# Kernel optimization log

Measured on AMD Instinct MI355X. Metric: run time of the kernel, lower is better.

Reference implementation:

```python
import jax, jax.numpy as jnp
import numpy as np

N_NODES = 100000
N_EDGES = 300000
D = 256
N_LAYERS = 9
LN_EPS = 1e-5


def _mlp(h, w1, b1, w2, b2, ln_g, ln_b):
    # torch Linear: y = x @ W.T + b ; W is [out, in]
    h = jax.nn.relu(jnp.einsum('nd,hd->nh', h, w1) + b1)
    h = jnp.einsum('nh,oh->no', h, w2) + b2
    mu = jnp.mean(h, axis=-1, keepdims=True)
    var = jnp.mean(jnp.square(h - mu), axis=-1, keepdims=True)
    return (h - mu) * jax.lax.rsqrt(var + LN_EPS) * ln_g + ln_b


def setup_inputs() -> dict:
    key = jax.random.key(0)
    ks = jax.random.split(key, 16)
    s = 0.05  # small init scale for numerical sanity across 9 layers
    inp = {
        'x': jax.random.normal(ks[0], (N_NODES, D), dtype=jnp.float32),
        'edge_attr': jax.random.normal(ks[1], (N_EDGES, D), dtype=jnp.float32),
        'edge_fc1_w': jax.random.normal(ks[2], (N_LAYERS, D, D), dtype=jnp.float32) * s,
        'edge_fc1_b': jnp.zeros((N_LAYERS, D), dtype=jnp.float32),
        'edge_fc2_w': jax.random.normal(ks[3], (N_LAYERS, D, D), dtype=jnp.float32) * s,
        'edge_fc2_b': jnp.zeros((N_LAYERS, D), dtype=jnp.float32),
        'edge_ln_g': jnp.ones((N_LAYERS, D), dtype=jnp.float32),
        'edge_ln_b': jnp.zeros((N_LAYERS, D), dtype=jnp.float32),
        'node_fc1_w': jax.random.normal(ks[4], (N_LAYERS, D, D), dtype=jnp.float32) * s,
        'node_fc1_b': jnp.zeros((N_LAYERS, D), dtype=jnp.float32),
        'node_fc2_w': jax.random.normal(ks[5], (N_LAYERS, D, D), dtype=jnp.float32) * s,
        'node_fc2_b': jnp.zeros((N_LAYERS, D), dtype=jnp.float32),
        'node_ln_g': jnp.ones((N_LAYERS, D), dtype=jnp.float32),
        'node_ln_b': jnp.zeros((N_LAYERS, D), dtype=jnp.float32),
        'edge_index': jax.random.randint(ks[6], (2, N_EDGES), 0, N_NODES, dtype=jnp.int32),
    }
    return inp


def reference(x, edge_attr, edge_fc1_w, edge_fc1_b, edge_fc2_w, edge_fc2_b,
              edge_ln_g, edge_ln_b, node_fc1_w, node_fc1_b, node_fc2_w, node_fc2_b,
              node_ln_g, node_ln_b, edge_index):
    src = edge_index[0]  # x_j
    tgt = edge_index[1]  # aggregation target (aggr='add')
    for l in range(N_LAYERS):
        # edge MLP is applied to the ORIGINAL edge_attr in every layer
        e = _mlp(edge_attr, edge_fc1_w[l], edge_fc1_b[l], edge_fc2_w[l], edge_fc2_b[l],
                 edge_ln_g[l], edge_ln_b[l])
        msg = x[src] + e                               # [E, D] gather + add
        aggr = jax.ops.segment_sum(msg, tgt, num_segments=N_NODES)  # scatter-add
        upd = _mlp(aggr, node_fc1_w[l], node_fc1_b[l], node_fc2_w[l], node_fc2_b[l],
                   node_ln_g[l], node_ln_b[l])
        x = upd + x                                    # residual
    return x
```

## Files before the change

### kernel.cpp

```cpp
#include <hip/hip_runtime.h>
#include <stdint.h>

#define DD 256
#define NEDGE 300000
#define NNODE 100000
#define NLAY 9
#define LN_EPS 1e-5f

typedef __attribute__((ext_vector_type(8))) short bf16x8;
typedef __attribute__((ext_vector_type(4))) short s16x4;
typedef __attribute__((ext_vector_type(4))) float f32x4;
typedef __attribute__((ext_vector_type(4))) int i32x4;

static __device__ __forceinline__ short f2bf(float f) {
  union { float f; uint32_t u; } v; v.f = f;
  uint32_t r = (v.u + 0x7FFFu + ((v.u >> 16) & 1u)) >> 16;
  return (short)(uint16_t)r;
}
static __device__ __forceinline__ float bf2f(short s) {
  union { uint32_t u; float f; } v; v.u = ((uint32_t)(uint16_t)s) << 16;
  return v.f;
}
static __device__ __forceinline__ int addbf2(int a, int b) {
  const float a0 = bf2f((short)(a & 0xffff)), a1 = bf2f((short)(((uint32_t)a) >> 16));
  const float b0 = bf2f((short)(b & 0xffff)), b1 = bf2f((short)(((uint32_t)b) >> 16));
  const uint16_t r0 = (uint16_t)f2bf(a0 + b0), r1 = (uint16_t)f2bf(a1 + b1);
  return (int)(((uint32_t)r1 << 16) | r0);
}

static __device__ __forceinline__ void gld16(const void* g, void* l) {
  __builtin_amdgcn_global_load_lds((const __attribute__((address_space(1))) void*)g,
                                   (__attribute__((address_space(3))) void*)l, 16, 0, 0);
}

__global__ void cvtw_kernel(const float* __restrict__ src, short* __restrict__ dst, int nmat) {
  const int total = nmat * 8192;
  for (int j = blockIdx.x * blockDim.x + threadIdx.x; j < total; j += gridDim.x * blockDim.x) {
    const int m = j >> 13;
    const int jj = j & 8191;
    const int col = jj & 255;
    const int kq = jj >> 8;
    const float* s = src + (size_t)m * 65536 + col * 256 + kq * 8;
    const f32x4 u0 = *(const f32x4*)(s);
    const f32x4 u1 = *(const f32x4*)(s + 4);
    bf16x8 o;
#pragma unroll
    for (int q = 0; q < 4; ++q) { o[q] = f2bf(u0[q]); o[q + 4] = f2bf(u1[q]); }
    *(bf16x8*)(dst + (size_t)j * 8) = o;
  }
}

template<bool A_BF16, bool NODE>
__global__ __launch_bounds__(512, 4) void mlp_kernel(
    const void* __restrict__ Ain, const int* __restrict__ rowmap,
    const short* __restrict__ W1t, const short* __restrict__ W2t,
    const float* __restrict__ B1, const float* __restrict__ B2,
    const float* __restrict__ LG, const float* __restrict__ LB,
    short* __restrict__ OutB, float* __restrict__ OutF,
    short* __restrict__ XbOut, int M) {
  extern __shared__ char smem[];
  char* Abuf = smem + 32768;
  float* redbuf = (float*)(smem + 65536);
  const int tid = threadIdx.x;
  const int lane = tid & 63;
  const int wv = tid >> 6;
  const int wm = wv >> 2, wn = wv & 3;
  const int l15 = lane & 15, lq = lane >> 4;
  const int cbase = wn * 64;
  const int r0 = blockIdx.x * 64;

  auto stageW = [&](const short* Wt, int s, int slot) {
#pragma unroll
    for (int j = 0; j < 2; ++j) {
      const int c = tid + 512 * j;
      gld16(Wt + ((size_t)s * 1024 + c) * 8, smem + slot * 16384 + c * 16);
    }
  };

  if (A_BF16) {
    const short* A = (const short*)Ain;
#pragma unroll
    for (int j = 0; j < 4; ++j) {
      const int c = tid + 512 * j;
      const int row = c & 63, kq = c >> 6;
      const int gr = min(r0 + row, M - 1);
      gld16(A + (size_t)gr * DD + kq * 8, Abuf + c * 16);
    }
  } else {
    const float* A = (const float*)Ain;
#pragma unroll
    for (int j = 0; j < 4; ++j) {
      const int c = tid + 512 * j;
      const int row = c & 63, kq = c >> 6;
      const int gr0 = min(r0 + row, M - 1);
      const int gr = rowmap ? rowmap[gr0] : gr0;
      const f32x4 u0 = *(const f32x4*)(A + (size_t)gr * DD + kq * 8);
      const f32x4 u1 = *(const f32x4*)(A + (size_t)gr * DD + kq * 8 + 4);
      bf16x8 o;
#pragma unroll
      for (int q = 0; q < 4; ++q) { o[q] = f2bf(u0[q]); o[q + 4] = f2bf(u1[q]); }
      *(bf16x8*)(Abuf + c * 16) = o;
    }
  }
  stageW(W1t, 0, 0);
  __syncthreads();

  f32x4 acc[2][4];
#pragma unroll
  for (int mi = 0; mi < 2; ++mi)
#pragma unroll
    for (int ni = 0; ni < 4; ++ni) acc[mi][ni] = (f32x4){0.f, 0.f, 0.f, 0.f};

#pragma unroll
  for (int s = 0; s < 8; ++s) {
    if (s < 7) stageW(W1t, s + 1, (s + 1) & 1);
    else       stageW(W2t, 0, 0);
    const char* wb = smem + (s & 1) * 16384;
    bf16x8 a[2], b[4];
#pragma unroll
    for (int mi = 0; mi < 2; ++mi)
      a[mi] = *(const bf16x8*)(Abuf + (((s * 4 + lq) * 64) + wm * 32 + mi * 16 + l15) * 16);
#pragma unroll
    for (int ni = 0; ni < 4; ++ni)
      b[ni] = *(const bf16x8*)(wb + lq * 4096 + (cbase + ni * 16 + l15) * 16);
#pragma unroll
    for (int ni = 0; ni < 4; ++ni)
#pragma unroll
      for (int mi = 0; mi < 2; ++mi)
        acc[mi][ni] = __builtin_amdgcn_mfma_f32_16x16x32_bf16(b[ni], a[mi], acc[mi][ni], 0, 0, 0);
    __syncthreads();
  }

  short* hid = (short*)Abuf;
  {
    f32x4 b1q[4];
#pragma unroll
    for (int ni = 0; ni < 4; ++ni)
      b1q[ni] = *(const f32x4*)(B1 + cbase + ni * 16 + lq * 4);
#pragma unroll
    for (int mi = 0; mi < 2; ++mi) {
      const int r = wm * 32 + mi * 16 + l15;
#pragma unroll
      for (int ni = 0; ni < 4; ++ni) {
        const int c4 = cbase + ni * 16 + lq * 4;
        s16x4 o;
#pragma unroll
        for (int i = 0; i < 4; ++i) {
          o[i] = f2bf(fmaxf(acc[mi][ni][i] + b1q[ni][i], 0.f));
          acc[mi][ni][i] = 0.f;
        }
        *(s16x4*)((char*)hid + r * 512 + (((c4 >> 3) ^ (r & 7)) << 4) + (c4 & 7) * 2) = o;
      }
    }
  }
  __syncthreads();

#pragma unroll
  for (int s = 0; s < 8; ++s) {
    if (s < 7) stageW(W2t, s + 1, (s + 1) & 1);
    const char* wb = smem + (s & 1) * 16384;
    bf16x8 a[2], b[4];
#pragma unroll
    for (int mi = 0; mi < 2; ++mi) {
      const int r = wm * 32 + mi * 16 + l15;
      a[mi] = *(const bf16x8*)((const char*)hid + r * 512 + ((((s * 4 + lq)) ^ (r & 7)) << 4));
    }
#pragma unroll
    for (int ni = 0; ni < 4; ++ni)
      b[ni] = *(const bf16x8*)(wb + lq * 4096 + (cbase + ni * 16 + l15) * 16);
#pragma unroll
    for (int ni = 0; ni < 4; ++ni)
#pragma unroll
      for (int mi = 0; mi < 2; ++mi)
        acc[mi][ni] = __builtin_amdgcn_mfma_f32_16x16x32_bf16(b[ni], a[mi], acc[mi][ni], 0, 0, 0);
    __syncthreads();
  }

  f32x4 b2q[4];
#pragma unroll
  for (int ni = 0; ni < 4; ++ni)
    b2q[ni] = *(const f32x4*)(B2 + cbase + ni * 16 + lq * 4);
  float mean_[2], inv_[2];
#pragma unroll
  for (int mi = 0; mi < 2; ++mi) {
    float s1 = 0.f, s2 = 0.f;
#pragma unroll
    for (int ni = 0; ni < 4; ++ni)
#pragma unroll
      for (int i = 0; i < 4; ++i) {
        const float v = acc[mi][ni][i] + b2q[ni][i];
        s1 += v; s2 += v * v;
      }
    s1 += __shfl_xor(s1, 16); s2 += __shfl_xor(s2, 16);
    s1 += __shfl_xor(s1, 32); s2 += __shfl_xor(s2, 32);
    mean_[mi] = s1; inv_[mi] = s2;
  }
  if (lq == 0) {
#pragma unroll
    for (int mi = 0; mi < 2; ++mi) {
      const int r = wm * 32 + mi * 16 + l15;
      redbuf[(r * 4 + wn) * 2 + 0] = mean_[mi];
      redbuf[(r * 4 + wn) * 2 + 1] = inv_[mi];
    }
  }
  __syncthreads();
#pragma unroll
  for (int mi = 0; mi < 2; ++mi) {
    const int r = wm * 32 + mi * 16 + l15;
    float t1 = 0.f, t2 = 0.f;
#pragma unroll
    for (int w = 0; w < 4; ++w) {
      t1 += redbuf[(r * 4 + w) * 2 + 0];
      t2 += redbuf[(r * 4 + w) * 2 + 1];
    }
    const float mean = t1 * (1.f / 256.f);
    const float var = t2 * (1.f / 256.f) - mean * mean;
    mean_[mi] = mean;
    inv_[mi] = rsqrtf(var + LN_EPS);
  }

  f32x4 gq[4], bq[4];
#pragma unroll
  for (int ni = 0; ni < 4; ++ni) {
    gq[ni] = *(const f32x4*)(LG + cbase + ni * 16 + lq * 4);
    bq[ni] = *(const f32x4*)(LB + cbase + ni * 16 + lq * 4);
  }

  if (NODE) {
    const bool wantF = (OutF != nullptr);
    if (!wantF) {
      short* ob = (short*)Abuf;
#pragma unroll
      for (int mi = 0; mi < 2; ++mi) {
        const int r = wm * 32 + mi * 16 + l15;
#pragma unroll
        for (int ni = 0; ni < 4; ++ni) {
          const int c4 = cbase + ni * 16 + lq * 4;
          s16x4 o;
#pragma unroll
          for (int i = 0; i < 4; ++i)
            o[i] = f2bf((acc[mi][ni][i] + b2q[ni][i] - mean_[mi]) * inv_[mi] * gq[ni][i] + bq[ni][i]);
          *(s16x4*)((char*)ob + r * 512 + (((c4 >> 3) ^ (r & 7)) << 4) + (c4 & 7) * 2) = o;
        }
      }
      __syncthreads();
#pragma unroll
      for (int j = 0; j < 4; ++j) {
        const int gg = tid + 512 * j;
        const int row = gg >> 5, Lg = gg & 31;
        const int grow = r0 + row;
        if (grow < M) {
          const i32x4 yv = *(const i32x4*)((const short*)ob + row * DD + ((Lg ^ (row & 7)) << 3));
          i32x4 xv = *(const i32x4*)(XbOut + (size_t)grow * DD + Lg * 8);
#pragma unroll
          for (int q = 0; q < 4; ++q) xv[q] = addbf2(yv[q], xv[q]);
          *(i32x4*)(XbOut + (size_t)grow * DD + Lg * 8) = xv;
        }
      }
    } else {
      float* ob = (float*)Abuf;
#pragma unroll
      for (int h = 0; h < 2; ++h) {
        if ((cbase >> 7) == h) {
#pragma unroll
          for (int mi = 0; mi < 2; ++mi) {
            const int r = wm * 32 + mi * 16 + l15;
#pragma unroll
            for (int ni = 0; ni < 4; ++ni) {
              const int cl4 = cbase - h * 128 + ni * 16 + lq * 4;
              f32x4 y;
#pragma unroll
              for (int i = 0; i < 4; ++i)
                y[i] = (acc[mi][ni][i] + b2q[ni][i] - mean_[mi]) * inv_[mi] * gq[ni][i] + bq[ni][i];
              *(f32x4*)((char*)ob + r * 512 + ((((cl4 >> 2) ^ (r & 7))) << 4)) = y;
            }
          }
        }
        __syncthreads();
#pragma unroll
        for (int j = 0; j < 4; ++j) {
          const int gg = tid + 512 * j;
          const int row = gg >> 5, Lc = gg & 31;
          const int grow = r0 + row;
          if (grow < M) {
            f32x4 v = *(const f32x4*)(ob + row * 128 + ((Lc ^ (row & 7)) << 2));
            const s16x4 xr = *(const s16x4*)(XbOut + (size_t)grow * DD + h * 128 + Lc * 4);
            v.x += bf2f(xr.x); v.y += bf2f(xr.y); v.z += bf2f(xr.z); v.w += bf2f(xr.w);
            *(f32x4*)(OutF + (size_t)grow * DD + h * 128 + Lc * 4) = v;
          }
        }
        if (h == 0) __syncthreads();
      }
    }
  } else {
    short* ob = (short*)Abuf;
#pragma unroll
    for (int mi = 0; mi < 2; ++mi) {
      const int r = wm * 32 + mi * 16 + l15;
#pragma unroll
      for (int ni = 0; ni < 4; ++ni) {
        const int c4 = cbase + ni * 16 + lq * 4;
        s16x4 o;
#pragma unroll
        for (int i = 0; i < 4; ++i)
          o[i] = f2bf((acc[mi][ni][i] + b2q[ni][i] - mean_[mi]) * inv_[mi] * gq[ni][i] + bq[ni][i]);
        *(s16x4*)((char*)ob + r * 512 + (((c4 >> 3) ^ (r & 7)) << 4) + (c4 & 7) * 2) = o;
      }
    }
    __syncthreads();
#pragma unroll
    for (int j = 0; j < 4; ++j) {
      const int gg = tid + 512 * j;
      const int row = gg >> 5, Lg = gg & 31;
      const int grow = r0 + row;
      if (grow < M) {
        const i32x4 v = *(const i32x4*)((const short*)ob + row * DD + ((Lg ^ (row & 7)) << 3));
        *(i32x4*)(OutB + (size_t)grow * DD + Lg * 8) = v;
      }
    }
  }
}

__global__ __launch_bounds__(256) void aggregate_kernel(
    const short* __restrict__ xb, const short* __restrict__ efs,
    const int* __restrict__ offs, const int* __restrict__ ssrc,
    short* __restrict__ aggr) {
  const int w = (blockIdx.x * blockDim.x + threadIdx.x) >> 6;
  if (w >= NNODE) return;
  const int lane = threadIdx.x & 63;
  const int beg = offs[w], end = offs[w + 1];
  float s0 = 0.f, s1 = 0.f, s2 = 0.f, s3 = 0.f;
  int p = beg;
  for (; p + 3 < end; p += 4) {
    const int a0 = ssrc[p], a1 = ssrc[p + 1], a2 = ssrc[p + 2], a3 = ssrc[p + 3];
    const s16x4 e0 = *(const s16x4*)(efs + (size_t)p * DD + lane * 4);
    const s16x4 e1 = *(const s16x4*)(efs + (size_t)(p + 1) * DD + lane * 4);
    const s16x4 e2 = *(const s16x4*)(efs + (size_t)(p + 2) * DD + lane * 4);
    const s16x4 e3 = *(const s16x4*)(efs + (size_t)(p + 3) * DD + lane * 4);
    const s16x4 x0 = *(const s16x4*)(xb + (size_t)a0 * DD + lane * 4);
    const s16x4 x1 = *(const s16x4*)(xb + (size_t)a1 * DD + lane * 4);
    const s16x4 x2 = *(const s16x4*)(xb + (size_t)a2 * DD + lane * 4);
    const s16x4 x3 = *(const s16x4*)(xb + (size_t)a3 * DD + lane * 4);
    s0 += bf2f(e0.x) + bf2f(x0.x) + bf2f(e1.x) + bf2f(x1.x) +
          bf2f(e2.x) + bf2f(x2.x) + bf2f(e3.x) + bf2f(x3.x);
    s1 += bf2f(e0.y) + bf2f(x0.y) + bf2f(e1.y) + bf2f(x1.y) +
          bf2f(e2.y) + bf2f(x2.y) + bf2f(e3.y) + bf2f(x3.y);
    s2 += bf2f(e0.z) + bf2f(x0.z) + bf2f(e1.z) + bf2f(x1.z) +
          bf2f(e2.z) + bf2f(x2.z) + bf2f(e3.z) + bf2f(x3.z);
    s3 += bf2f(e0.w) + bf2f(x0.w) + bf2f(e1.w) + bf2f(x1.w) +
          bf2f(e2.w) + bf2f(x2.w) + bf2f(e3.w) + bf2f(x3.w);
  }
  for (; p < end; ++p) {
    const s16x4 ev = *(const s16x4*)(efs + (size_t)p * DD + lane * 4);
    const s16x4 xv = *(const s16x4*)(xb + (size_t)ssrc[p] * DD + lane * 4);
    s0 += bf2f(ev.x) + bf2f(xv.x);
    s1 += bf2f(ev.y) + bf2f(xv.y);
    s2 += bf2f(ev.z) + bf2f(xv.z);
    s3 += bf2f(ev.w) + bf2f(xv.w);
  }
  s16x4 o; o.x = f2bf(s0); o.y = f2bf(s1); o.z = f2bf(s2); o.w = f2bf(s3);
  *(s16x4*)(aggr + (size_t)w * DD + lane * 4) = o;
}

__global__ void count_kernel(const int* __restrict__ tgt, int* __restrict__ deg) {
  const int e = blockIdx.x * 256 + threadIdx.x;
  if (e < NEDGE) atomicAdd(&deg[tgt[e]], 1);
}

__global__ __launch_bounds__(256) void scan1_kernel(
    const int* __restrict__ deg, int* __restrict__ locex, int* __restrict__ bsum) {
  __shared__ int sh[256];
  const int t = threadIdx.x, b = blockIdx.x;
  const int idx = b * 256 + t;
  const int v = (idx < NNODE) ? deg[idx] : 0;
  sh[t] = v;
  __syncthreads();
#pragma unroll
  for (int off = 1; off < 256; off <<= 1) {
    const int add = (t >= off) ? sh[t - off] : 0;
    __syncthreads();
    sh[t] += add;
    __syncthreads();
  }
  if (idx < NNODE) locex[idx] = sh[t] - v;
  if (t == 255) bsum[b] = sh[255];
}

__global__ __launch_bounds__(512) void scan2_kernel(int* __restrict__ bsum, int nb) {
  __shared__ int sh[512];
  const int t = threadIdx.x;
  const int v = (t < nb) ? bsum[t] : 0;
  sh[t] = v;
  __syncthreads();
#pragma unroll
  for (int off = 1; off < 512; off <<= 1) {
    const int add = (t >= off) ? sh[t - off] : 0;
    __syncthreads();
    sh[t] += add;
    __syncthreads();
  }
  if (t < nb) bsum[t] = sh[t] - v;
}

__global__ __launch_bounds__(256) void scan3_kernel(
    const int* __restrict__ locex, const int* __restrict__ bsum,
    int* __restrict__ offs, int* __restrict__ cur) {
  const int idx = blockIdx.x * 256 + threadIdx.x;
  if (idx < NNODE) {
    const int o = locex[idx] + bsum[blockIdx.x];
    offs[idx] = o;
    cur[idx] = o;
  }
  if (idx == 0) offs[NNODE] = NEDGE;
}

__global__ void fill_kernel(const int* __restrict__ src, const int* __restrict__ tgt,
                            int* cur, int* seid, int* ssrc) {
  const int e = blockIdx.x * 256 + threadIdx.x;
  if (e < NEDGE) {
    const int t = tgt[e];
    const int p = atomicAdd(&cur[t], 1);
    seid[p] = e;
    ssrc[p] = src[e];
  }
}

__global__ void cvt4_kernel(const float* __restrict__ src, short* __restrict__ dst, int n4) {
  for (int i = blockIdx.x * blockDim.x + threadIdx.x; i < n4; i += gridDim.x * blockDim.x) {
    const f32x4 v = ((const f32x4*)src)[i];
    s16x4 o;
    o.x = f2bf(v.x); o.y = f2bf(v.y); o.z = f2bf(v.z); o.w = f2bf(v.w);
    ((s16x4*)dst)[i] = o;
  }
}

__global__ __launch_bounds__(256) void gather_cvt_kernel(
    const float* __restrict__ src, const int* __restrict__ perm,
    short* __restrict__ dst, int n) {
  const int w = (blockIdx.x * blockDim.x + threadIdx.x) >> 6;
  if (w >= n) return;
  const int lane = threadIdx.x & 63;
  const f32x4 v = *(const f32x4*)(src + (size_t)perm[w] * DD + lane * 4);
  s16x4 o; o.x = f2bf(v.x); o.y = f2bf(v.y); o.z = f2bf(v.z); o.w = f2bf(v.w);
  *(s16x4*)(dst + (size_t)w * DD + lane * 4) = o;
}

extern "C" void kernel_launch(void* const* d_in, const int* in_sizes, int n_in,
                              void* d_out, int out_size, void* d_ws, size_t ws_size,
                              hipStream_t stream) {
  const float* x_in = (const float*)d_in[0];
  const float* ea_f = (const float*)d_in[1];
  const float* e1w = (const float*)d_in[2];
  const float* e1b = (const float*)d_in[3];
  const float* e2w = (const float*)d_in[4];
  const float* e2b = (const float*)d_in[5];
  const float* elg = (const float*)d_in[6];
  const float* elb = (const float*)d_in[7];
  const float* n1w = (const float*)d_in[8];
  const float* n1b = (const float*)d_in[9];
  const float* n2w = (const float*)d_in[10];
  const float* n2b = (const float*)d_in[11];
  const float* nlg = (const float*)d_in[12];
  const float* nlb = (const float*)d_in[13];
  const int* eidx = (const int*)d_in[14];
  float* x = (float*)d_out;

  char* p = (char*)d_ws;
  auto take = [&](size_t bytes) {
    char* r = p;
    p += (bytes + 255) & ~(size_t)255;
    return r;
  };
  short* efeat = (short*)take((size_t)NEDGE * DD * 2);
  short* aggr = (short*)take((size_t)NNODE * DD * 2);
  short* xb = (short*)take((size_t)NNODE * DD * 2);
  short* we1t = (short*)take((size_t)NLAY * DD * DD * 2);
  short* we2t = (short*)take((size_t)NLAY * DD * DD * 2);
  short* wn1t = (short*)take((size_t)NLAY * DD * DD * 2);
  short* wn2t = (short*)take((size_t)NLAY * DD * DD * 2);
  int* deg = (int*)take((size_t)NNODE * 4);
  int* offs = (int*)take((size_t)(NNODE + 1) * 4);
  int* cur = (int*)take((size_t)NNODE * 4);
  int* seid = (int*)take((size_t)NEDGE * 4);
  int* ssrc = (int*)take((size_t)NEDGE * 4);
  int* locex = (int*)take((size_t)(NNODE + 256) * 4);
  int* bsum = (int*)take(512 * 4);
  short* eab = (short*)take((size_t)NEDGE * DD * 2);
  const bool use_eab = ((size_t)(p - (char*)d_ws) <= ws_size);

  const int SMEM = 67584;
  hipFuncSetAttribute((const void*)mlp_kernel<true, false>,
                      hipFuncAttributeMaxDynamicSharedMemorySize, SMEM);
  hipFuncSetAttribute((const void*)mlp_kernel<false, false>,
                      hipFuncAttributeMaxDynamicSharedMemorySize, SMEM);
  hipFuncSetAttribute((const void*)mlp_kernel<true, true>,
                      hipFuncAttributeMaxDynamicSharedMemorySize, SMEM);

  cvtw_kernel<<<288, 256, 0, stream>>>(e1w, we1t, NLAY);
  cvtw_kernel<<<288, 256, 0, stream>>>(e2w, we2t, NLAY);
  cvtw_kernel<<<288, 256, 0, stream>>>(n1w, wn1t, NLAY);
  cvtw_kernel<<<288, 256, 0, stream>>>(n2w, wn2t, NLAY);
  cvt4_kernel<<<2048, 256, 0, stream>>>(x_in, xb, NNODE * DD / 4);

  const int NB = (NNODE + 255) / 256;
  hipMemsetAsync(deg, 0, (size_t)NNODE * 4, stream);
  count_kernel<<<(NEDGE + 255) / 256, 256, 0, stream>>>(eidx + NEDGE, deg);
  scan1_kernel<<<NB, 256, 0, stream>>>(deg, locex, bsum);
  scan2_kernel<<<1, 512, 0, stream>>>(bsum, NB);
  scan3_kernel<<<NB, 256, 0, stream>>>(locex, bsum, offs, cur);
  fill_kernel<<<(NEDGE + 255) / 256, 256, 0, stream>>>(eidx, eidx + NEDGE, cur, seid, ssrc);
  if (use_eab)
    gather_cvt_kernel<<<NEDGE / 4, 256, 0, stream>>>(ea_f, seid, eab, NEDGE);

  const int egrid = (NEDGE + 63) / 64;
  const int ngrid = (NNODE + 63) / 64;
  for (int l = 0; l < NLAY; ++l) {
    if (use_eab) {
      mlp_kernel<true, false><<<egrid, 512, SMEM, stream>>>(
          eab, nullptr, we1t + l * 65536, we2t + l * 65536, e1b + l * DD,
          e2b + l * DD, elg + l * DD, elb + l * DD, efeat, nullptr,
          nullptr, NEDGE);
    } else {
      mlp_kernel<false, false><<<egrid, 512, SMEM, stream>>>(
          ea_f, seid, we1t + l * 65536, we2t + l * 65536, e1b + l * DD,
          e2b + l * DD, elg + l * DD, elb + l * DD, efeat, nullptr,
          nullptr, NEDGE);
    }
    aggregate_kernel<<<(NNODE * 64 + 255) / 256, 256, 0, stream>>>(xb, efeat, offs, ssrc, aggr);
    mlp_kernel<true, true><<<ngrid, 512, SMEM, stream>>>(
        aggr, nullptr, wn1t + l * 65536, wn2t + l * 65536, n1b + l * DD,
        n2b + l * DD, nlg + l * DD, nlb + l * DD, nullptr,
        (l == NLAY - 1) ? x : nullptr, xb, NNODE);
  }
  (void)in_sizes; (void)n_in; (void)out_size; (void)ws_size;
}
```

Before: 2.632 ms.

## Fuse neighbor aggregation into node MLP kernel with ping-pong node buffers

Removes the separate aggregate kernel and performs the gather-sum of edge features plus source node features inside the node MLP kernel's A-tile load, writing directly to shared memory. Node feature buffers are double-buffered so blocks can read neighbors' old features while writing updated ones. This avoids writing and re-reading the aggregated tensor and a launch per layer, but the per-thread-per-row gather has poorer coalescing and divergent degree loops inside a heavy MLP block.

```diff
diff --git a/kernel.cpp b/kernel.cpp
--- a/kernel.cpp
+++ b/kernel.cpp
@@ -53,6 +53,8 @@
 template<bool A_BF16, bool NODE>
 __global__ __launch_bounds__(512, 4) void mlp_kernel(
     const void* __restrict__ Ain, const int* __restrict__ rowmap,
+    const int* __restrict__ offs, const int* __restrict__ ssrc,
+    const short* __restrict__ XbIn,
     const short* __restrict__ W1t, const short* __restrict__ W2t,
     const float* __restrict__ B1, const float* __restrict__ B2,
     const float* __restrict__ LG, const float* __restrict__ LB,
@@ -77,7 +79,39 @@
     }
   };
 
-  if (A_BF16) {
+  stageW(W1t, 0, 0);
+
+  if (NODE) {
+    const short* efs = (const short*)Ain;
+    const int r = tid & 63;
+    const int j = tid >> 6;
+    const int n = min(r0 + r, M - 1);
+    const int beg = offs[n], end = offs[n + 1];
+    float s[4][8];
+#pragma unroll
+    for (int c = 0; c < 4; ++c)
+#pragma unroll
+      for (int q = 0; q < 8; ++q) s[c][q] = 0.f;
+    for (int p = beg; p < end; ++p) {
+      const int src = ssrc[p];
+#pragma unroll
+      for (int c = 0; c < 4; ++c) {
+        const int kq = j * 4 + c;
+        const bf16x8 ev = *(const bf16x8*)(efs + (size_t)p * DD + kq * 8);
+        const bf16x8 xv = *(const bf16x8*)(XbIn + (size_t)src * DD + kq * 8);
+#pragma unroll
+        for (int q = 0; q < 8; ++q) s[c][q] += bf2f(ev[q]) + bf2f(xv[q]);
+      }
+    }
+#pragma unroll
+    for (int c = 0; c < 4; ++c) {
+      const int kq = j * 4 + c;
+      bf16x8 o;
+#pragma unroll
+      for (int q = 0; q < 8; ++q) o[q] = f2bf(s[c][q]);
+      *(bf16x8*)(Abuf + (kq * 64 + r) * 16) = o;
+    }
+  } else if (A_BF16) {
     const short* A = (const short*)Ain;
 #pragma unroll
     for (int j = 0; j < 4; ++j) {
@@ -102,7 +136,6 @@
       *(bf16x8*)(Abuf + c * 16) = o;
     }
   }
-  stageW(W1t, 0, 0);
   __syncthreads();
 
   f32x4 acc[2][4];
@@ -251,7 +284,7 @@
         const int grow = r0 + row;
         if (grow < M) {
           const i32x4 yv = *(const i32x4*)((const short*)ob + row * DD + ((Lg ^ (row & 7)) << 3));
-          i32x4 xv = *(const i32x4*)(XbOut + (size_t)grow * DD + Lg * 8);
+          i32x4 xv = *(const i32x4*)(XbIn + (size_t)grow * DD + Lg * 8);
 #pragma unroll
           for (int q = 0; q < 4; ++q) xv[q] = addbf2(yv[q], xv[q]);
           *(i32x4*)(XbOut + (size_t)grow * DD + Lg * 8) = xv;
@@ -284,7 +317,7 @@
           const int grow = r0 + row;
           if (grow < M) {
             f32x4 v = *(const f32x4*)(ob + row * 128 + ((Lc ^ (row & 7)) << 2));
-            const s16x4 xr = *(const s16x4*)(XbOut + (size_t)grow * DD + h * 128 + Lc * 4);
+            const s16x4 xr = *(const s16x4*)(XbIn + (size_t)grow * DD + h * 128 + Lc * 4);
             v.x += bf2f(xr.x); v.y += bf2f(xr.y); v.z += bf2f(xr.z); v.w += bf2f(xr.w);
             *(f32x4*)(OutF + (size_t)grow * DD + h * 128 + Lc * 4) = v;
           }
@@ -319,47 +352,6 @@
       }
     }
   }
-}
-
-__global__ __launch_bounds__(256) void aggregate_kernel(
-    const short* __restrict__ xb, const short* __restrict__ efs,
-    const int* __restrict__ offs, const int* __restrict__ ssrc,
-    short* __restrict__ aggr) {
-  const int w = (blockIdx.x * blockDim.x + threadIdx.x) >> 6;
-  if (w >= NNODE) return;
-  const int lane = threadIdx.x & 63;
-  const int beg = offs[w], end = offs[w + 1];
-  float s0 = 0.f, s1 = 0.f, s2 = 0.f, s3 = 0.f;
-  int p = beg;
-  for (; p + 3 < end; p += 4) {
-    const int a0 = ssrc[p], a1 = ssrc[p + 1], a2 = ssrc[p + 2], a3 = ssrc[p + 3];
-    const s16x4 e0 = *(const s16x4*)(efs + (size_t)p * DD + lane * 4);
-    const s16x4 e1 = *(const s16x4*)(efs + (size_t)(p + 1) * DD + lane * 4);
-    const s16x4 e2 = *(const s16x4*)(efs + (size_t)(p + 2) * DD + lane * 4);
-    const s16x4 e3 = *(const s16x4*)(efs + (size_t)(p + 3) * DD + lane * 4);
-    const s16x4 x0 = *(const s16x4*)(xb + (size_t)a0 * DD + lane * 4);
-    const s16x4 x1 = *(const s16x4*)(xb + (size_t)a1 * DD + lane * 4);
-    const s16x4 x2 = *(const s16x4*)(xb + (size_t)a2 * DD + lane * 4);
-    const s16x4 x3 = *(const s16x4*)(xb + (size_t)a3 * DD + lane * 4);
-    s0 += bf2f(e0.x) + bf2f(x0.x) + bf2f(e1.x) + bf2f(x1.x) +
-          bf2f(e2.x) + bf2f(x2.x) + bf2f(e3.x) + bf2f(x3.x);
-    s1 += bf2f(e0.y) + bf2f(x0.y) + bf2f(e1.y) + bf2f(x1.y) +
-          bf2f(e2.y) + bf2f(x2.y) + bf2f(e3.y) + bf2f(x3.y);
-    s2 += bf2f(e0.z) + bf2f(x0.z) + bf2f(e1.z) + bf2f(x1.z) +
-          bf2f(e2.z) + bf2f(x2.z) + bf2f(e3.z) + bf2f(x3.z);
-    s3 += bf2f(e0.w) + bf2f(x0.w) + bf2f(e1.w) + bf2f(x1.w) +
-          bf2f(e2.w) + bf2f(x2.w) + bf2f(e3.w) + bf2f(x3.w);
-  }
-  for (; p < end; ++p) {
-    const s16x4 ev = *(const s16x4*)(efs + (size_t)p * DD + lane * 4);
-    const s16x4 xv = *(const s16x4*)(xb + (size_t)ssrc[p] * DD + lane * 4);
-    s0 += bf2f(ev.x) + bf2f(xv.x);
-    s1 += bf2f(ev.y) + bf2f(xv.y);
-    s2 += bf2f(ev.z) + bf2f(xv.z);
-    s3 += bf2f(ev.w) + bf2f(xv.w);
-  }
-  s16x4 o; o.x = f2bf(s0); o.y = f2bf(s1); o.z = f2bf(s2); o.w = f2bf(s3);
-  *(s16x4*)(aggr + (size_t)w * DD + lane * 4) = o;
 }
 
 __global__ void count_kernel(const int* __restrict__ tgt, int* __restrict__ deg) {
@@ -472,8 +464,8 @@
     return r;
   };
   short* efeat = (short*)take((size_t)NEDGE * DD * 2);
-  short* aggr = (short*)take((size_t)NNODE * DD * 2);
-  short* xb = (short*)take((size_t)NNODE * DD * 2);
+  short* xbA = (short*)take((size_t)NNODE * DD * 2);
+  short* xbB = (short*)take((size_t)NNODE * DD * 2);
   short* we1t = (short*)take((size_t)NLAY * DD * DD * 2);
   short* we2t = (short*)take((size_t)NLAY * DD * DD * 2);
   short* wn1t = (short*)take((size_t)NLAY * DD * DD * 2);
@@ -500,7 +492,7 @@
   cvtw_kernel<<<288, 256, 0, stream>>>(e2w, we2t, NLAY);
   cvtw_kernel<<<288, 256, 0, stream>>>(n1w, wn1t, NLAY);
   cvtw_kernel<<<288, 256, 0, stream>>>(n2w, wn2t, NLAY);
-  cvt4_kernel<<<2048, 256, 0, stream>>>(x_in, xb, NNODE * DD / 4);
+  cvt4_kernel<<<2048, 256, 0, stream>>>(x_in, xbA, NNODE * DD / 4);
 
   const int NB = (NNODE + 255) / 256;
   hipMemsetAsync(deg, 0, (size_t)NNODE * 4, stream);
@@ -514,23 +506,28 @@
 
   const int egrid = (NEDGE + 63) / 64;
   const int ngrid = (NNODE + 63) / 64;
+  short* xin = xbA;
+  short* xout = xbB;
   for (int l = 0; l < NLAY; ++l) {
     if (use_eab) {
       mlp_kernel<true, false><<<egrid, 512, SMEM, stream>>>(
-          eab, nullptr, we1t + l * 65536, we2t + l * 65536, e1b + l * DD,
+          eab, nullptr, nullptr, nullptr, nullptr,
+          we1t + l * 65536, we2t + l * 65536, e1b + l * DD,
           e2b + l * DD, elg + l * DD, elb + l * DD, efeat, nullptr,
           nullptr, NEDGE);
     } else {
       mlp_kernel<false, false><<<egrid, 512, SMEM, stream>>>(
-          ea_f, seid, we1t + l * 65536, we2t + l * 65536, e1b + l * DD,
+          ea_f, seid, nullptr, nullptr, nullptr,
+          we1t + l * 65536, we2t + l * 65536, e1b + l * DD,
           e2b + l * DD, elg + l * DD, elb + l * DD, efeat, nullptr,
           nullptr, NEDGE);
     }
-    aggregate_kernel<<<(NNODE * 64 + 255) / 256, 256, 0, stream>>>(xb, efeat, offs, ssrc, aggr);
     mlp_kernel<true, true><<<ngrid, 512, SMEM, stream>>>(
-        aggr, nullptr, wn1t + l * 65536, wn2t + l * 65536, n1b + l * DD,
+        efeat, nullptr, offs, ssrc, xin,
+        wn1t + l * 65536, wn2t + l * 65536, n1b + l * DD,
         n2b + l * DD, nlg + l * DD, nlb + l * DD, nullptr,
-        (l == NLAY - 1) ? x : nullptr, xb, NNODE);
+        (l == NLAY - 1) ? x : nullptr, xout, NNODE);
+    short* t = xin; xin = xout; xout = t;
   }
   (void)in_sizes; (void)n_in; (void)out_size; (void)ws_size;
 }
```

Measured after the change: 2.579 ms. 1.02x faster.
